# Optimization experiments

Measured on AMD Instinct MI355X. Metric: run time of the kernel, lower is better.

Reference implementation:

```python
import jax, jax.numpy as jnp
import numpy as np

PC_RANGE = [-51.2, -51.2, -5.0, 51.2, 51.2, 3.0]
NUM_HEADS, NUM_LEVELS, NUM_REFS, NUM_POINTS = 8, 4, 4, 1
EPS = 1e-5


def setup_inputs():
    key = jax.random.key(0)
    ks = jax.random.split(key, 16)
    B, CAMS, NQ, C, R = 1, 6, 10000, 256, NUM_REFS
    H, L, P = NUM_HEADS, NUM_LEVELS, NUM_POINTS
    shapes = np.array([[64, 160], [32, 80], [16, 40], [8, 20]], dtype=np.int64)
    hw = shapes[:, 0] * shapes[:, 1]
    lsi = np.concatenate([[0], np.cumsum(hw)[:-1]]).astype(np.int64)
    NK = int(hw.sum())

    def p(k, shape):
        return 0.02 * jax.random.normal(k, shape, jnp.float32)

    return {
        'query': jax.random.normal(ks[0], (NQ, B, C), jnp.float32),
        'query_pos': jax.random.normal(ks[1], (NQ, B, C), jnp.float32),
        'value': jax.random.normal(ks[2], (NK, B * CAMS, C), jnp.float32),
        'bev_reference_points': jax.random.uniform(ks[3], (B, NQ, R, 3), jnp.float32),
        'lidar2img': jax.random.normal(ks[4], (B, CAMS, 3, 4), jnp.float32),
        'img_shape': jnp.broadcast_to(jnp.array([512.0, 960.0], jnp.float32), (B, CAMS, 2)),
        'spatial_shapes': jnp.asarray(shapes),
        'level_start_index': jnp.asarray(lsi),
        'W_val': p(ks[5], (C, C)), 'b_val': jnp.zeros((C,), jnp.float32),
        'W_samp': p(ks[6], (C, H * L * R * P * 2)), 'b_samp': p(ks[7], (H * L * R * P * 2,)),
        'W_attn': p(ks[8], (C, H * L * R * P)), 'b_attn': jnp.zeros((H * L * R * P,), jnp.float32),
        'W_dout': p(ks[9], (C, C)), 'b_dout': jnp.zeros((C,), jnp.float32),
        'W_out': p(ks[10], (C, C)), 'b_out': jnp.zeros((C,), jnp.float32),
    }


def reference(query, query_pos, value, bev_reference_points, lidar2img, img_shape,
              spatial_shapes, level_start_index,
              W_val, b_val, W_samp, b_samp, W_attn, b_attn, W_dout, b_dout, W_out, b_out):
    shapes = np.asarray(spatial_shapes)
    lsi = np.asarray(level_start_index)
    H, L, R, P = NUM_HEADS, NUM_LEVELS, NUM_REFS, NUM_POINTS
    identity = query                                   # (NQ,B,C)
    q = jnp.transpose(query + query_pos, (1, 0, 2))    # (B,NQ,C)
    v = jnp.transpose(value, (1, 0, 2))                # (Bc,NK,C)
    B, NQ, C = q.shape
    CAMS = lidar2img.shape[1]
    Bc, dh = B * CAMS, C // H
    pc = jnp.asarray(PC_RANGE, q.dtype)

    # ---- project 3D reference points to each camera ----
    l2i = jnp.zeros((B, CAMS, 4, 4), q.dtype).at[..., 3, 3].set(1.0).at[..., :3, :4].set(lidar2img)
    xyz = bev_reference_points * (pc[3:6] - pc[0:3]) + pc[0:3]          # (B,NQ,R,3)
    pts = jnp.concatenate([xyz, jnp.ones_like(xyz[..., :1])], -1).reshape(B, NQ * R, 4)
    cam = jnp.einsum('bcij,bnj->bcni', l2i, pts)                         # (B,CAMS,NQ*R,4)
    z = cam[..., 2]
    xy = cam[..., :2] / jnp.maximum(z, EPS)[..., None]
    xy = xy / img_shape[:, :, None, ::-1]                                # x/w, y/h
    mask = (z > EPS) & (xy[..., 0] > 0.) & (xy[..., 0] < 1.) & (xy[..., 1] > 0.) & (xy[..., 1] < 1.)
    mask = mask.reshape(B, CAMS, NQ, R)
    ref_cam = xy.reshape(B, CAMS, NQ, R, 2)

    # rebatch: run attention for all queries per camera, mask outputs (same math as
    # gather-only-valid since deformable attention is pointwise per query)
    q_rb = jnp.broadcast_to(q[:, None], (B, CAMS, NQ, C)).reshape(Bc, NQ, C)
    rp_rb = ref_cam.reshape(Bc, NQ, R, 2)

    # ---- multi-scale deformable attention ----
    vproj = jnp.transpose((v @ W_val + b_val).reshape(Bc, -1, H, dh), (0, 2, 1, 3))  # (Bc,H,NK,dh)
    off = (q_rb @ W_samp + b_samp).reshape(Bc, NQ, H, L, R, P, 2)
    aw = jax.nn.softmax((q_rb @ W_attn + b_attn).reshape(Bc, NQ, H, L * R * P), -1)
    aw = aw.reshape(Bc, NQ, H, L, R, P)
    norm = jnp.asarray(shapes[:, ::-1].copy(), q.dtype)                  # (L,2) = (w,h)
    loc = rp_rb[:, :, None, None, :, None, :] + off / norm[None, None, None, :, None, None, :]

    acc = jnp.zeros((Bc, H, NQ, dh), q.dtype)
    for l in range(L):
        Hl, Wl, s = int(shapes[l, 0]), int(shapes[l, 1]), int(lsi[l])
        vf = vproj[:, :, s:s + Hl * Wl]                                  # (Bc,H,Hl*Wl,dh)

        def rs(t):  # (Bc,NQ,H,R,P) -> (Bc,H,M)
            return jnp.transpose(t, (0, 2, 1, 3, 4)).reshape(Bc, H, NQ * R * P)
        x = rs(loc[:, :, :, l, :, :, 0]) * Wl - 0.5   # grid_sample align_corners=False
        y = rs(loc[:, :, :, l, :, :, 1]) * Hl - 0.5
        w = rs(aw[:, :, :, l])
        x0 = jnp.floor(x); y0 = jnp.floor(y)
        lx = x - x0; ly = y - y0
        ix = x0.astype(jnp.int32); iy = y0.astype(jnp.int32)

        def g(iy_, ix_):  # zero-padding gather
            inb = (iy_ >= 0) & (iy_ < Hl) & (ix_ >= 0) & (ix_ < Wl)
            idx = jnp.clip(iy_, 0, Hl - 1) * Wl + jnp.clip(ix_, 0, Wl - 1)
            return jnp.take_along_axis(vf, idx[..., None], axis=2) * inb[..., None].astype(q.dtype)
        samp = (g(iy, ix) * ((1 - ly) * (1 - lx) * w)[..., None]
                + g(iy, ix + 1) * ((1 - ly) * lx * w)[..., None]
                + g(iy + 1, ix) * (ly * (1 - lx) * w)[..., None]
                + g(iy + 1, ix + 1) * (ly * lx * w)[..., None])            # (Bc,H,M,dh)
        acc = acc + samp.reshape(Bc, H, NQ, R * P, dh).sum(3)
    attn_out = jnp.transpose(acc, (0, 2, 1, 3)).reshape(Bc, NQ, C) @ W_dout + b_dout

    # ---- scatter/average valid camera contributions back to BEV slots ----
    valid = jnp.any(mask, -1)                                            # (B,CAMS,NQ)
    slots = jnp.sum(attn_out.reshape(B, CAMS, NQ, C) * valid[..., None].astype(q.dtype), 1)
    count = jnp.maximum(valid.sum(1).astype(q.dtype), 1.0)               # (B,NQ)
    slots = (slots / count[..., None]) @ W_out + b_out
    return jnp.transpose(slots, (1, 0, 2)) + identity
```

## Files before the change

### kernel.cpp

```cpp
#include <hip/hip_runtime.h>
#include <hip/hip_bf16.h>

namespace {

typedef unsigned short u16;
typedef unsigned int u32;
typedef unsigned char u8;
typedef __attribute__((ext_vector_type(8))) short bf16x8;
typedef __attribute__((ext_vector_type(4))) float f32x4;
typedef __attribute__((ext_vector_type(2))) float f32x2;

constexpr int kNQ   = 10000;
constexpr int kCams = 6;
constexpr int kC    = 256;
constexpr int kNK   = 13600;
constexpr float kEps = 1e-5f;

__device__ __forceinline__ u16 f2b(float f) {
  union { __hip_bfloat16 h; u16 u; } cv;
  cv.h = __float2bfloat16(f);
  return cv.u;
}
__device__ __forceinline__ float b2f(u16 b) {
  return __uint_as_float(((u32)b) << 16);
}
__device__ __forceinline__ bf16x8 pack8(const float4& a, const float4& b) {
  bf16x8 v;
  v[0] = (short)f2b(a.x); v[1] = (short)f2b(a.y);
  v[2] = (short)f2b(a.z); v[3] = (short)f2b(a.w);
  v[4] = (short)f2b(b.x); v[5] = (short)f2b(b.y);
  v[6] = (short)f2b(b.z); v[7] = (short)f2b(b.w);
  return v;
}
__device__ __forceinline__ bf16x8 cvt8(const f32x4 lo, const f32x4 hi) {
  bf16x8 v;
  v[0] = (short)f2b(lo[0]); v[1] = (short)f2b(lo[1]);
  v[2] = (short)f2b(lo[2]); v[3] = (short)f2b(lo[3]);
  v[4] = (short)f2b(hi[0]); v[5] = (short)f2b(hi[1]);
  v[6] = (short)f2b(hi[2]); v[7] = (short)f2b(hi[3]);
  return v;
}
__device__ __forceinline__ u8 f2fp8(float v) {
  const u32 t = __builtin_amdgcn_cvt_pk_fp8_f32(v, 0.f, 0u, false);
  return (u8)(t & 0xffu);
}
__device__ __forceinline__ void gload16(const void* g, void* l) {
  __builtin_amdgcn_global_load_lds(
      (const __attribute__((address_space(1))) void*)g,
      (__attribute__((address_space(3))) void*)l, 16, 0, 0);
}

__global__ __launch_bounds__(256) void k_cvt_w_all(
    const float* __restrict__ w_val, const float* __restrict__ w_samp,
    const float* __restrict__ w_attn, const float* __restrict__ w_dout,
    const float* __restrict__ w_out, u16* __restrict__ t_val,
    u16* __restrict__ t_sa, u16* __restrict__ t_dout, u16* __restrict__ t_out) {
  __shared__ float t[32][33];
  const int bn = blockIdx.x;
  const int bk = blockIdx.y;
  const int tid = threadIdx.x;
  const float* W; u16* Wt; int N, lb;
  if (bn < 8)       { W = w_val;  Wt = t_val;            N = 256; lb = bn; }
  else if (bn < 16) { W = w_samp; Wt = t_sa;             N = 256; lb = bn - 8; }
  else if (bn < 20) { W = w_attn; Wt = t_sa + 256 * 256; N = 128; lb = bn - 16; }
  else if (bn < 28) { W = w_dout; Wt = t_dout;           N = 256; lb = bn - 20; }
  else              { W = w_out;  Wt = t_out;            N = 256; lb = bn - 28; }
#pragma unroll
  for (int e = 0; e < 4; ++e) {
    const int i = e * 256 + tid;
    const int kk = i >> 5, nn = i & 31;
    t[kk][nn] = W[(bk * 32 + kk) * N + lb * 32 + nn];
  }
  __syncthreads();
#pragma unroll
  for (int e = 0; e < 4; ++e) {
    const int i = e * 256 + tid;
    const int nn = i >> 5, kk = i & 31;
    Wt[(lb * 32 + nn) * 256 + bk * 32 + kk] = f2b(t[kk][nn]);
  }
}

__global__ __launch_bounds__(256) void k_cvt_add(const float* __restrict__ a,
                                                 const float* __restrict__ b,
                                                 u16* __restrict__ out) {
  const int t = blockIdx.x * 256 + threadIdx.x;
  const int i = t * 8;
  const float4 x0 = *reinterpret_cast<const float4*>(a + i);
  const float4 x1 = *reinterpret_cast<const float4*>(a + i + 4);
  const float4 y0 = *reinterpret_cast<const float4*>(b + i);
  const float4 y1 = *reinterpret_cast<const float4*>(b + i + 4);
  float4 s0, s1;
  s0.x = x0.x + y0.x; s0.y = x0.y + y0.y; s0.z = x0.z + y0.z; s0.w = x0.w + y0.w;
  s1.x = x1.x + y1.x; s1.y = x1.y + y1.y; s1.z = x1.z + y1.z; s1.w = x1.w + y1.w;
  *reinterpret_cast<bf16x8*>(out + i) = pack8(s0, s1);
}

template <bool OUT_BF16, bool HAS_ADD>
__global__ __launch_bounds__(256) void k_mfma(const u16* __restrict__ A,
                                              const u16* __restrict__ Wt,
                                              const float* __restrict__ bias,
                                              const float* __restrict__ bias2,
                                              int nsplit,
                                              const float* __restrict__ bias_scale,
                                              const float* __restrict__ addend,
                                              void* __restrict__ outp,
                                              int M, int Ntot) {
  __shared__ u16 As[128 * 64];
  __shared__ u16 Bs[128 * 64];
  const int tid = threadIdx.x;
  const int m0 = blockIdx.x * 128;
  const int n0 = blockIdx.y * 128;
  const int wave = tid >> 6;
  const int lane = tid & 63;
  const int wr = wave >> 1;
  const int wc = wave & 1;
  const int lr = lane & 15;
  const int lg = lane >> 4;
  const int srow = tid >> 3;
  const int slot = tid & 7;

  const u16* aptr[4];
  const u16* bptr[4];
  int soff[4];
#pragma unroll
  for (int c = 0; c < 4; ++c) {
    const int rowA = c * 32 + srow;
    const int ra = min(m0 + rowA, M - 1);
    aptr[c] = A + (long long)ra * 256 + slot * 8;
    bptr[c] = Wt + (long long)(n0 + rowA) * 256 + slot * 8;
    soff[c] = rowA * 64 + ((slot ^ (rowA & 7)) << 3);
  }

  f32x4 acc[4][4] = {};

  bf16x8 ca[4], cb[4];
#pragma unroll
  for (int c = 0; c < 4; ++c) {
    ca[c] = *reinterpret_cast<const bf16x8*>(aptr[c]);
    cb[c] = *reinterpret_cast<const bf16x8*>(bptr[c]);
  }

#pragma unroll
  for (int kt = 0; kt < 4; ++kt) {
    bf16x8 na[4], nb[4];
    if (kt < 3) {
      const int k1 = (kt + 1) * 64;
#pragma unroll
      for (int c = 0; c < 4; ++c) {
        na[c] = *reinterpret_cast<const bf16x8*>(aptr[c] + k1);
        nb[c] = *reinterpret_cast<const bf16x8*>(bptr[c] + k1);
      }
    }
#pragma unroll
    for (int c = 0; c < 4; ++c) {
      *reinterpret_cast<bf16x8*>(&As[soff[c]]) = ca[c];
      *reinterpret_cast<bf16x8*>(&Bs[soff[c]]) = cb[c];
    }
    __syncthreads();
#pragma unroll
    for (int ks = 0; ks < 2; ++ks) {
      bf16x8 af[4], bfr[4];
#pragma unroll
      for (int mi = 0; mi < 4; ++mi) {
        const int r = wr * 64 + mi * 16 + lr;
        const int s = ks * 4 + lg;
        af[mi] = *reinterpret_cast<const bf16x8*>(&As[r * 64 + ((s ^ (r & 7)) << 3)]);
      }
#pragma unroll
      for (int ni = 0; ni < 4; ++ni) {
        const int r = wc * 64 + ni * 16 + lr;
        const int s = ks * 4 + lg;
        bfr[ni] = *reinterpret_cast<const bf16x8*>(&Bs[r * 64 + ((s ^ (r & 7)) << 3)]);
      }
#pragma unroll
      for (int mi = 0; mi < 4; ++mi)
#pragma unroll
        for (int ni = 0; ni < 4; ++ni)
          acc[mi][ni] = __builtin_amdgcn_mfma_f32_16x16x32_bf16(af[mi], bfr[ni],
                                                                acc[mi][ni], 0, 0, 0);
    }
    if (kt < 3) {
      __syncthreads();
#pragma unroll
      for (int c = 0; c < 4; ++c) { ca[c] = na[c]; cb[c] = nb[c]; }
    }
  }

#pragma unroll
  for (int mi = 0; mi < 4; ++mi) {
#pragma unroll
    for (int reg = 0; reg < 4; ++reg) {
      const int row = m0 + wr * 64 + mi * 16 + lg * 4 + reg;
      if (row < M) {
        const float bs = bias_scale ? bias_scale[row] : 1.f;
#pragma unroll
        for (int ni = 0; ni < 4; ++ni) {
          const int col = n0 + wc * 64 + ni * 16 + lr;
          const float b = (bias2 && col >= nsplit) ? bias2[col - nsplit] : bias[col];
          float v = acc[mi][ni][reg] + b * bs;
          if (HAS_ADD) v += addend[(long long)row * Ntot + col];
          if (OUT_BF16)
            ((u16*)outp)[(long long)row * Ntot + col] = f2b(v);
          else
            ((float*)outp)[(long long)row * Ntot + col] = v;
        }
      }
    }
  }
}

__global__ __launch_bounds__(512, 4) void k_mfma_vproj(
    const float* __restrict__ value, const u16* __restrict__ Wt,
    const float* __restrict__ bias, u8* __restrict__ outp) {
  constexpr int M = kNK * kCams;
  __shared__ float AsF[2][128 * 32];
  __shared__ u16  BsH[2][256 * 32];
  const int tid = threadIdx.x;
  const int m0 = blockIdx.x * 128;
  const int wid = tid >> 6;
  const int lane = tid & 63;
  const int wrow = wid >> 1;
  const int wcol = wid & 1;
  const int lr = lane & 15;
  const int lg = lane >> 4;

  const float* asrc[2];
#pragma unroll
  for (int i = 0; i < 2; ++i) {
    const int r = i * 64 + (tid >> 3);
    const int g = min(m0 + r, M - 1);
    const int cam = g / kNK;
    const int n = g - cam * kNK;
    const int cs = (tid & 7) ^ (r & 7);
    asrc[i] = value + (long long)(n * kCams + cam) * 256 + cs * 4;
  }
  const u16* bsrc[2];
#pragma unroll
  for (int j = 0; j < 2; ++j) {
    const int rb = j * 128 + (tid >> 2);
    const int cs = (tid & 3) ^ ((rb >> 1) & 3);
    bsrc[j] = Wt + (long long)rb * 256 + cs * 8;
  }

  f32x4 acc[2][8] = {};

#pragma unroll
  for (int i = 0; i < 2; ++i)
    gload16(asrc[i], (char*)(&AsF[0][0]) + i * 8192 + wid * 1024);
#pragma unroll
  for (int j = 0; j < 2; ++j)
    gload16(bsrc[j], (char*)(&BsH[0][0]) + j * 8192 + wid * 1024);
  __syncthreads();

  for (int kt = 0; kt < 8; ++kt) {
    const int buf = kt & 1;
    if (kt < 7) {
      const int ko = (kt + 1) * 32;
#pragma unroll
      for (int i = 0; i < 2; ++i)
        gload16(asrc[i] + ko, (char*)(&AsF[buf ^ 1][0]) + i * 8192 + wid * 1024);
#pragma unroll
      for (int j = 0; j < 2; ++j)
        gload16(bsrc[j] + ko, (char*)(&BsH[buf ^ 1][0]) + j * 8192 + wid * 1024);
    }
    const float* Ab = &AsF[buf][0];
    const u16* Bb = &BsH[buf][0];
    bf16x8 af[2];
#pragma unroll
    for (int mi = 0; mi < 2; ++mi) {
      const int r = wrow * 32 + mi * 16 + lr;
      const int c0 = (lg * 2) ^ (r & 7);
      const int c1 = (lg * 2 + 1) ^ (r & 7);
      const f32x4 lo = *reinterpret_cast<const f32x4*>(Ab + r * 32 + c0 * 4);
      const f32x4 hi = *reinterpret_cast<const f32x4*>(Ab + r * 32 + c1 * 4);
      af[mi] = cvt8(lo, hi);
    }
    bf16x8 bfr[8];
#pragma unroll
    for (int ni = 0; ni < 8; ++ni) {
      const int rb = wcol * 128 + ni * 16 + lr;
      const int c = lg ^ ((rb >> 1) & 3);
      bfr[ni] = *reinterpret_cast<const bf16x8*>(Bb + rb * 32 + c * 8);
    }
#pragma unroll
    for (int mi = 0; mi < 2; ++mi)
#pragma unroll
      for (int ni = 0; ni < 8; ++ni)
        acc[mi][ni] = __builtin_amdgcn_mfma_f32_16x16x32_bf16(af[mi], bfr[ni],
                                                              acc[mi][ni], 0, 0, 0);
    __syncthreads();
  }

#pragma unroll
  for (int mi = 0; mi < 2; ++mi) {
#pragma unroll
    for (int reg = 0; reg < 4; ++reg) {
      const int row = m0 + wrow * 32 + mi * 16 + lg * 4 + reg;
      if (row < M) {
#pragma unroll
        for (int ni = 0; ni < 8; ++ni) {
          const int col = wcol * 128 + ni * 16 + lr;
          outp[(long long)row * 256 + col] = f2fp8(acc[mi][ni][reg] + bias[col]);
        }
      }
    }
  }
}

__global__ __launch_bounds__(128) void k_softmax16(float* __restrict__ offaw) {
  const int nq = blockIdx.x;
  const int t = threadIdx.x;
  float* p = offaw + (long long)nq * 384 + 256 + t;
  float v = *p;
  float mx = v;
#pragma unroll
  for (int s = 1; s < 16; s <<= 1) mx = fmaxf(mx, __shfl_xor(mx, s));
  const float e = expf(v - mx);
  float sm = e;
#pragma unroll
  for (int s = 1; s < 16; s <<= 1) sm += __shfl_xor(sm, s);
  *p = e / sm;
}

__global__ __launch_bounds__(256) void k_proj_ref(const float* __restrict__ refpts,
                                                  const float* __restrict__ l2i,
                                                  const float* __restrict__ img_shape,
                                                  float* __restrict__ refcam,
                                                  float* __restrict__ valid) {
  const int idx = blockIdx.x * blockDim.x + threadIdx.x;
  if (idx >= kCams * kNQ) return;
  const int cam = idx / kNQ;
  const int nq = idx - cam * kNQ;
  const float* Mp = l2i + cam * 12;
  float m[12];
#pragma unroll
  for (int i = 0; i < 12; ++i) m[i] = Mp[i];
  const float ih = img_shape[cam * 2 + 0];
  const float iw = img_shape[cam * 2 + 1];
  float anyv = 0.f;
  float* rcout = refcam + (long long)idx * 8;
#pragma unroll
  for (int r = 0; r < 4; ++r) {
    const float* rp = refpts + ((long long)nq * 4 + r) * 3;
    const float X = rp[0] * 102.4f + (-51.2f);
    const float Y = rp[1] * 102.4f + (-51.2f);
    const float Z = rp[2] * 8.0f + (-5.0f);
    const float cx = m[0] * X + m[1] * Y + m[2] * Z + m[3];
    const float cy = m[4] * X + m[5] * Y + m[6] * Z + m[7];
    const float cz = m[8] * X + m[9] * Y + m[10] * Z + m[11];
    const float zc = fmaxf(cz, kEps);
    const float xn = cx / zc / iw;
    const float yn = cy / zc / ih;
    rcout[r * 2 + 0] = xn;
    rcout[r * 2 + 1] = yn;
    if ((cz > kEps) && (xn > 0.f) && (xn < 1.f) && (yn > 0.f) && (yn < 1.f)) anyv = 1.f;
  }
  valid[idx] = anyv;
}

__global__ __launch_bounds__(64) void k_sample(const u8* __restrict__ vproj,
                                               const float* __restrict__ refcam,
                                               const float* __restrict__ offaw,
                                               const float* __restrict__ valid,
                                               u16* __restrict__ pre,
                                               float* __restrict__ cflag) {
  const int nq = blockIdx.x;
  const int lane = threadIdx.x;
  const int h = lane >> 3;
  const int d4 = lane & 7;

  static constexpr int SHH[4] = {64, 32, 16, 8};
  static constexpr int SHW[4] = {160, 80, 40, 20};
  static constexpr int LSI[4] = {0, 10240, 12800, 13440};

  const float* offp = offaw + (long long)nq * 384 + h * 32;
  const float* awp = offaw + (long long)nq * 384 + 256 + h * 16;

  float vl[kCams];
#pragma unroll
  for (int c = 0; c < kCams; ++c) vl[c] = valid[c * kNQ + nq];

  float4 acc4 = {0.f, 0.f, 0.f, 0.f};
  float count = 0.f;

  for (int cam = 0; cam < kCams; ++cam) {
    if (vl[cam] == 0.f) continue;
    count += 1.f;

    const float* rcp = refcam + (long long)(cam * kNQ + nq) * 8;
    const float4 rcA = *reinterpret_cast<const float4*>(rcp);
    const float4 rcB = *reinterpret_cast<const float4*>(rcp + 4);
    const float rx[4] = {rcA.x, rcA.z, rcB.x, rcB.z};
    const float ry[4] = {rcA.y, rcA.w, rcB.y, rcB.w};

#pragma unroll
    for (int l = 0; l < 4; ++l) {
      const int Hl = SHH[l];
      const int Wl = SHW[l];
      const float Hf = (float)Hl;
      const float Wf = (float)Wl;
      const float4 aw4 = *reinterpret_cast<const float4*>(awp + l * 4);
      const float4 ofA = *reinterpret_cast<const float4*>(offp + l * 8);
      const float4 ofB = *reinterpret_cast<const float4*>(offp + l * 8 + 4);
      const u8* vf = vproj + ((long long)(cam * kNK + LSI[l])) * 256 + h * 32 + d4 * 4;

      const float ox[4] = {ofA.x, ofA.z, ofB.x, ofB.z};
      const float oy[4] = {ofA.y, ofA.w, ofB.y, ofB.w};
      const float wr[4] = {aw4.x, aw4.y, aw4.z, aw4.w};

#pragma unroll
      for (int r = 0; r < 4; ++r) {
        const float x = fmaf(rx[r], Wf, ox[r]) - 0.5f;
        const float y = fmaf(ry[r], Hf, oy[r]) - 0.5f;
        const float x0 = floorf(x);
        const float y0 = floorf(y);
        const float lx = x - x0;
        const float ly = y - y0;
        const int ix = (int)x0;
        const int iy = (int)y0;
        const int ix0 = min(max(ix, 0), Wl - 1);
        const int ix1 = min(max(ix + 1, 0), Wl - 1);
        const int iy0 = min(max(iy, 0), Hl - 1);
        const int iy1 = min(max(iy + 1, 0), Hl - 1);
        const bool bx0 = (ix >= 0) & (ix < Wl);
        const bool bx1 = (ix >= -1) & (ix + 1 < Wl);
        const bool by0 = (iy >= 0) & (iy < Hl);
        const bool by1 = (iy >= -1) & (iy + 1 < Hl);
        const float w = wr[r];
        const float wy0 = w * (1.f - ly);
        const float wy1 = w * ly;
        const float w00 = (by0 && bx0) ? wy0 * (1.f - lx) : 0.f;
        const float w01 = (by0 && bx1) ? wy0 * lx : 0.f;
        const float w10 = (by1 && bx0) ? wy1 * (1.f - lx) : 0.f;
        const float w11 = (by1 && bx1) ? wy1 * lx : 0.f;
        const int q00 = *reinterpret_cast<const u32*>(vf + (iy0 * Wl + ix0) * 256);
        const int q01 = *reinterpret_cast<const u32*>(vf + (iy0 * Wl + ix1) * 256);
        const int q10 = *reinterpret_cast<const u32*>(vf + (iy1 * Wl + ix0) * 256);
        const int q11 = *reinterpret_cast<const u32*>(vf + (iy1 * Wl + ix1) * 256);
        const f32x2 a00 = __builtin_amdgcn_cvt_pk_f32_fp8(q00, false);
        const f32x2 b00 = __builtin_amdgcn_cvt_pk_f32_fp8(q00, true);
        const f32x2 a01 = __builtin_amdgcn_cvt_pk_f32_fp8(q01, false);
        const f32x2 b01 = __builtin_amdgcn_cvt_pk_f32_fp8(q01, true);
        const f32x2 a10 = __builtin_amdgcn_cvt_pk_f32_fp8(q10, false);
        const f32x2 b10 = __builtin_amdgcn_cvt_pk_f32_fp8(q10, true);
        const f32x2 a11 = __builtin_amdgcn_cvt_pk_f32_fp8(q11, false);
        const f32x2 b11 = __builtin_amdgcn_cvt_pk_f32_fp8(q11, true);
        acc4.x = fmaf(w00, a00[0], fmaf(w01, a01[0], fmaf(w10, a10[0], fmaf(w11, a11[0], acc4.x))));
        acc4.y = fmaf(w00, a00[1], fmaf(w01, a01[1], fmaf(w10, a10[1], fmaf(w11, a11[1], acc4.y))));
        acc4.z = fmaf(w00, b00[0], fmaf(w01, b01[0], fmaf(w10, b10[0], fmaf(w11, b11[0], acc4.z))));
        acc4.w = fmaf(w00, b00[1], fmaf(w01, b01[1], fmaf(w10, b10[1], fmaf(w11, b11[1], acc4.w))));
      }
    }
  }

  const float inv = count > 0.f ? (1.f / count) : 0.f;
  ushort4 o;
  o.x = f2b(acc4.x * inv);
  o.y = f2b(acc4.y * inv);
  o.z = f2b(acc4.z * inv);
  o.w = f2b(acc4.w * inv);
  *reinterpret_cast<ushort4*>(pre + (long long)nq * kC + h * 32 + d4 * 4) = o;
  if (lane == 0) cflag[nq] = count > 0.f ? 1.f : 0.f;
}

}

extern "C" void kernel_launch(void* const* d_in, const int* in_sizes, int n_in,
                              void* d_out, int out_size, void* d_ws, size_t ws_size,
                              hipStream_t stream) {
  (void)in_sizes; (void)n_in; (void)out_size; (void)ws_size;
  const float* query     = (const float*)d_in[0];
  const float* query_pos = (const float*)d_in[1];
  const float* value     = (const float*)d_in[2];
  const float* refpts    = (const float*)d_in[3];
  const float* l2i       = (const float*)d_in[4];
  const float* img_shape = (const float*)d_in[5];
  const float* W_val  = (const float*)d_in[8];
  const float* b_val  = (const float*)d_in[9];
  const float* W_samp = (const float*)d_in[10];
  const float* b_samp = (const float*)d_in[11];
  const float* W_attn = (const float*)d_in[12];
  const float* b_attn = (const float*)d_in[13];
  const float* W_dout = (const float*)d_in[14];
  const float* b_dout = (const float*)d_in[15];
  const float* W_out  = (const float*)d_in[16];
  const float* b_out  = (const float*)d_in[17];

  char* p = (char*)d_ws;
  float* offaw  = (float*)p;  p += 15360000;
  float* refcam = (float*)p;  p += 1920000;
  float* valid  = (float*)p;  p += 240000;
  float* cflag  = (float*)p;  p += 40000;
  u8*    vproj  = (u8*)p;     p += 20889600;
  u16*   pre    = (u16*)p;    p += 5120000;
  u16*   slots  = (u16*)p;    p += 5120000;
  u16*   qpq    = (u16*)p;    p += 5120000;
  u16*   WtVal  = (u16*)p;    p += 131072;
  u16*   WtSA   = (u16*)p;    p += 196608;
  u16*   WtDout = (u16*)p;    p += 131072;
  u16*   WtOut  = (u16*)p;    p += 131072;
  float* out    = (float*)d_out;

  k_cvt_w_all<<<dim3(36, 8), 256, 0, stream>>>(W_val, W_samp, W_attn, W_dout, W_out,
                                               WtVal, WtSA, WtDout, WtOut);

  k_cvt_add<<<dim3(1250), 256, 0, stream>>>(query, query_pos, qpq);

  k_proj_ref<<<dim3((kCams * kNQ + 255) / 256), 256, 0, stream>>>(refpts, l2i,
                                                                  img_shape, refcam,
                                                                  valid);

  k_mfma<false, false><<<dim3(79, 3), 256, 0, stream>>>(
      qpq, WtSA, b_samp, b_attn, 256, nullptr, nullptr, offaw, kNQ, 384);
  k_softmax16<<<dim3(kNQ), 128, 0, stream>>>(offaw);

  k_mfma_vproj<<<dim3(638), 512, 0, stream>>>(value, WtVal, b_val, vproj);

  k_sample<<<dim3(kNQ), 64, 0, stream>>>(vproj, refcam, offaw, valid, pre, cflag);

  k_mfma<true, false><<<dim3(79, 2), 256, 0, stream>>>(
      pre, WtDout, b_dout, nullptr, 0, cflag, nullptr, slots, kNQ, 256);

  k_mfma<false, true><<<dim3(79, 2), 256, 0, stream>>>(
      slots, WtOut, b_out, nullptr, 0, nullptr, query, out, kNQ, 256);
}
```

Baseline: 124.2 us.

## Make value projection persistent with whole weight resident in LDS

The value-projection GEMM now runs as 256 persistent blocks. Each block loads the full 256x256 bf16 weight matrix into shared memory once and loops over row tiles, prefetching the next tile's fp32 activations into registers directly from global memory, so there is no LDS staging of A and no per-k-step barriers. Rows are read in the value tensor's natural order and the camera/key permutation is applied on the output store instead. The cost is 128KB of LDS per block and high register pressure from 16 prefetched vectors and 16 accumulators, which limits occupancy. Output writes are scattered single bytes.

```diff
diff --git a/kernel.cpp b/kernel.cpp
--- a/kernel.cpp
+++ b/kernel.cpp
@@ -209,99 +209,81 @@
   }
 }
 
-__global__ __launch_bounds__(512, 4) void k_mfma_vproj(
+__global__ __launch_bounds__(512, 2) void k_mfma_vproj(
     const float* __restrict__ value, const u16* __restrict__ Wt,
-    const float* __restrict__ bias, u8* __restrict__ outp) {
+    const float* __restrict__ bias, u8* __restrict__ outp, int ntiles) {
   constexpr int M = kNK * kCams;
-  __shared__ float AsF[2][128 * 32];
-  __shared__ u16  BsH[2][256 * 32];
+  __shared__ u16 B[256 * 256];
   const int tid = threadIdx.x;
-  const int m0 = blockIdx.x * 128;
-  const int wid = tid >> 6;
-  const int lane = tid & 63;
-  const int wrow = wid >> 1;
-  const int wcol = wid & 1;
-  const int lr = lane & 15;
-  const int lg = lane >> 4;
-
-  const float* asrc[2];
-#pragma unroll
-  for (int i = 0; i < 2; ++i) {
-    const int r = i * 64 + (tid >> 3);
-    const int g = min(m0 + r, M - 1);
-    const int cam = g / kNK;
-    const int n = g - cam * kNK;
-    const int cs = (tid & 7) ^ (r & 7);
-    asrc[i] = value + (long long)(n * kCams + cam) * 256 + cs * 4;
-  }
-  const u16* bsrc[2];
-#pragma unroll
-  for (int j = 0; j < 2; ++j) {
-    const int rb = j * 128 + (tid >> 2);
-    const int cs = (tid & 3) ^ ((rb >> 1) & 3);
-    bsrc[j] = Wt + (long long)rb * 256 + cs * 8;
-  }
-
-  f32x4 acc[2][8] = {};
-
-#pragma unroll
-  for (int i = 0; i < 2; ++i)
-    gload16(asrc[i], (char*)(&AsF[0][0]) + i * 8192 + wid * 1024);
-#pragma unroll
-  for (int j = 0; j < 2; ++j)
-    gload16(bsrc[j], (char*)(&BsH[0][0]) + j * 8192 + wid * 1024);
+  const int w = tid >> 6;
+  const int l = tid & 63;
+  const int lr = l & 15;
+  const int lg = l >> 4;
+  const int rb7 = lr & 7;
+
+#pragma unroll
+  for (int j = 0; j < 16; ++j) {
+    const int rb = j * 16 + w * 2 + (l >> 5);
+    const int p = l & 31;
+    gload16(Wt + rb * 256 + ((p ^ (rb & 7)) << 3),
+            (char*)B + j * 8192 + w * 1024 + l * 16);
+  }
+
+  float bcol[16];
+#pragma unroll
+  for (int ni = 0; ni < 16; ++ni) bcol[ni] = bias[ni * 16 + lr];
+
+  int tg = blockIdx.x;
+  f32x4 araw[16];
+  {
+    const int row = min(tg * 128 + w * 16 + lr, M - 1);
+    const float* ap = value + (long long)row * 256 + lg * 8;
+#pragma unroll
+    for (int ks = 0; ks < 8; ++ks) {
+      araw[2 * ks]     = *reinterpret_cast<const f32x4*>(ap + ks * 32);
+      araw[2 * ks + 1] = *reinterpret_cast<const f32x4*>(ap + ks * 32 + 4);
+    }
+  }
   __syncthreads();
 
-  for (int kt = 0; kt < 8; ++kt) {
-    const int buf = kt & 1;
-    if (kt < 7) {
-      const int ko = (kt + 1) * 32;
-#pragma unroll
-      for (int i = 0; i < 2; ++i)
-        gload16(asrc[i] + ko, (char*)(&AsF[buf ^ 1][0]) + i * 8192 + wid * 1024);
-#pragma unroll
-      for (int j = 0; j < 2; ++j)
-        gload16(bsrc[j] + ko, (char*)(&BsH[buf ^ 1][0]) + j * 8192 + wid * 1024);
-    }
-    const float* Ab = &AsF[buf][0];
-    const u16* Bb = &BsH[buf][0];
-    bf16x8 af[2];
-#pragma unroll
-    for (int mi = 0; mi < 2; ++mi) {
-      const int r = wrow * 32 + mi * 16 + lr;
-      const int c0 = (lg * 2) ^ (r & 7);
-      const int c1 = (lg * 2 + 1) ^ (r & 7);
-      const f32x4 lo = *reinterpret_cast<const f32x4*>(Ab + r * 32 + c0 * 4);
-      const f32x4 hi = *reinterpret_cast<const f32x4*>(Ab + r * 32 + c1 * 4);
-      af[mi] = cvt8(lo, hi);
-    }
-    bf16x8 bfr[8];
-#pragma unroll
-    for (int ni = 0; ni < 8; ++ni) {
-      const int rb = wcol * 128 + ni * 16 + lr;
-      const int c = lg ^ ((rb >> 1) & 3);
-      bfr[ni] = *reinterpret_cast<const bf16x8*>(Bb + rb * 32 + c * 8);
-    }
-#pragma unroll
-    for (int mi = 0; mi < 2; ++mi)
-#pragma unroll
-      for (int ni = 0; ni < 8; ++ni)
-        acc[mi][ni] = __builtin_amdgcn_mfma_f32_16x16x32_bf16(af[mi], bfr[ni],
-                                                              acc[mi][ni], 0, 0, 0);
-    __syncthreads();
-  }
-
-#pragma unroll
-  for (int mi = 0; mi < 2; ++mi) {
+  for (; tg < ntiles; tg += 256) {
+    bf16x8 af[8];
+#pragma unroll
+    for (int ks = 0; ks < 8; ++ks) af[ks] = cvt8(araw[2 * ks], araw[2 * ks + 1]);
+
+    const int tn = tg + 256;
+    if (tn < ntiles) {
+      const int row = min(tn * 128 + w * 16 + lr, M - 1);
+      const float* ap = value + (long long)row * 256 + lg * 8;
+#pragma unroll
+      for (int ks = 0; ks < 8; ++ks) {
+        araw[2 * ks]     = *reinterpret_cast<const f32x4*>(ap + ks * 32);
+        araw[2 * ks + 1] = *reinterpret_cast<const f32x4*>(ap + ks * 32 + 4);
+      }
+    }
+
+    f32x4 acc[16] = {};
+#pragma unroll
+    for (int ks = 0; ks < 8; ++ks) {
+#pragma unroll
+      for (int ni = 0; ni < 16; ++ni) {
+        const bf16x8 bf = *reinterpret_cast<const bf16x8*>(
+            (const char*)B + ni * 8192 + lr * 512 + (((ks * 4 + lg) ^ rb7) << 4));
+        acc[ni] = __builtin_amdgcn_mfma_f32_16x16x32_bf16(af[ks], bf, acc[ni],
+                                                          0, 0, 0);
+      }
+    }
+
 #pragma unroll
     for (int reg = 0; reg < 4; ++reg) {
-      const int row = m0 + wrow * 32 + mi * 16 + lg * 4 + reg;
+      const int row = tg * 128 + w * 16 + lg * 4 + reg;
       if (row < M) {
-#pragma unroll
-        for (int ni = 0; ni < 8; ++ni) {
-          const int col = wcol * 128 + ni * 16 + lr;
-          outp[(long long)row * 256 + col] = f2fp8(acc[mi][ni][reg] + bias[col]);
-        }
+        const u32 n = (u32)row / 6u;
+        const u32 cam = (u32)row - n * 6u;
+        u8* op = outp + ((long long)(cam * kNK + n)) * 256 + lr;
+#pragma unroll
+        for (int ni = 0; ni < 16; ++ni)
+          op[ni * 16] = f2fp8(acc[ni][reg] + bcol[ni]);
       }
     }
   }
@@ -514,7 +496,7 @@
       qpq, WtSA, b_samp, b_attn, 256, nullptr, nullptr, offaw, kNQ, 384);
   k_softmax16<<<dim3(kNQ), 128, 0, stream>>>(offaw);
 
-  k_mfma_vproj<<<dim3(638), 512, 0, stream>>>(value, WtVal, b_val, vproj);
+  k_mfma_vproj<<<dim3(256), 512, 0, stream>>>(value, WtVal, b_val, vproj, 638);
 
   k_sample<<<dim3(kNQ), 64, 0, stream>>>(vproj, refcam, offaw, valid, pre, cflag);
 
```

After: 328.3 us. 164% more time.
